# Optimization experiments

Measured on AMD Instinct MI355X. Metric: run time of the kernel, lower is better.

Reference implementation:

```python
import jax, jax.numpy as jnp
import numpy as np
from functools import partial

EPS = 1e-8

@partial(jax.custom_vjp, nondiff_argnums=(2, 3))
def ste_quantize(x, scale, clamp_min, clamp_max):
    # forward: clamp(round(x/scale), min, max); backward: grad/scale (STE)
    return jnp.clip(jnp.round(x / scale), clamp_min, clamp_max)

def _ste_fwd(x, scale, clamp_min, clamp_max):
    return ste_quantize(x, scale, clamp_min, clamp_max), scale

def _ste_bwd(clamp_min, clamp_max, scale, g):
    return (g / scale, jnp.zeros_like(scale))

ste_quantize.defvjp(_ste_fwd, _ste_bwd)


def setup_inputs() -> dict:
    key = jax.random.key(0)
    kx, kw = jax.random.split(key)
    x = jax.random.normal(kx, (4, 4096, 2048), dtype=jnp.float32)
    # nn.init.normal_(weight, mean=0.0, std=0.006)
    weight = 0.006 * jax.random.normal(kw, (2048, 2048), dtype=jnp.float32)
    return {"x": x, "weight": weight}


def reference(x, weight):
    # per-tensor ternary weight quantization: alpha = mean(|W|)
    alpha = jnp.maximum(jnp.mean(jnp.abs(weight)), EPS)
    w_q = ste_quantize(weight, alpha, -1.0, 1.0)  # (out, in), values in {-1,0,1}
    # per-token int8 activation quantization: beta = max(|x|)/127
    beta = jnp.maximum(jnp.max(jnp.abs(x), axis=-1, keepdims=True) / 127.0, EPS)  # (b,s,1)
    x_q = ste_quantize(x, beta, -127.0, 127.0)  # (b,s,in)
    # fp32 GEMM on quantized values, then dequant rescale
    y = jnp.einsum('bsi,oi->bso', x_q, w_q)
    return y * alpha * beta
```

## Files before the change

kernel.cpp:

```cpp
#include <hip/hip_runtime.h>

#define IN_DIM 2048
#define OUT_DIM 2048
#define EPS 1e-8f

#define BK 128
#define NKT (IN_DIM / BK)
#define HALF 16384

using int32x4 = __attribute__((ext_vector_type(4))) int;

__global__ __launch_bounds__(256) void prep_kernel(const float* __restrict__ x,
                                                   signed char* __restrict__ xq,
                                                   float* __restrict__ beta_arr,
                                                   int tokens,
                                                   const float* __restrict__ w,
                                                   double* __restrict__ sum, int n4) {
    if (blockIdx.x < 4096) {
        const int lane = threadIdx.x & 63;
        const int wave = threadIdx.x >> 6;
        const int t = blockIdx.x * 4 + wave;
        if (t >= tokens) return;
        const float4* row = (const float4*)(x + (size_t)t * IN_DIM);
        float4 v[8];
        float m = 0.f;
#pragma unroll
        for (int j = 0; j < 8; ++j) {
            v[j] = row[lane + 64 * j];
            m = fmaxf(m, fmaxf(fmaxf(fabsf(v[j].x), fabsf(v[j].y)),
                               fmaxf(fabsf(v[j].z), fabsf(v[j].w))));
        }
#pragma unroll
        for (int off = 32; off; off >>= 1) m = fmaxf(m, __shfl_xor(m, off));
        const float beta = fmaxf(m * (1.f / 127.f), EPS);
        if (lane == 0) beta_arr[t] = beta;
        char4* orow = (char4*)(xq + (size_t)t * IN_DIM);
#pragma unroll
        for (int j = 0; j < 8; ++j) {
            char4 q;
            q.x = (signed char)fminf(fmaxf(rintf(v[j].x / beta), -127.f), 127.f);
            q.y = (signed char)fminf(fmaxf(rintf(v[j].y / beta), -127.f), 127.f);
            q.z = (signed char)fminf(fmaxf(rintf(v[j].z / beta), -127.f), 127.f);
            q.w = (signed char)fminf(fmaxf(rintf(v[j].w / beta), -127.f), 127.f);
            orow[lane + 64 * j] = q;
        }
    } else {
        int tid = (blockIdx.x - 4096) * blockDim.x + threadIdx.x;
        int stride = 1024 * blockDim.x;
        float s = 0.f;
        for (int i = tid; i < n4; i += stride) {
            float4 vv = ((const float4*)w)[i];
            s += fabsf(vv.x) + fabsf(vv.y) + fabsf(vv.z) + fabsf(vv.w);
        }
        for (int off = 32; off; off >>= 1) s += __shfl_down(s, off);
        __shared__ float wsum[4];
        int lane = threadIdx.x & 63, wave = threadIdx.x >> 6;
        if (lane == 0) wsum[wave] = s;
        __syncthreads();
        if (threadIdx.x == 0) {
            double tt = (double)wsum[0] + (double)wsum[1] + (double)wsum[2] + (double)wsum[3];
            atomicAdd(sum, tt);
        }
    }
}

__global__ __launch_bounds__(256) void quantw_kernel(const float* __restrict__ w,
                                                     const double* __restrict__ sumptr,
                                                     signed char* __restrict__ wq,
                                                     float* __restrict__ alpha_out, int n4) {
    float alpha = fmaxf((float)(*sumptr * (1.0 / (double)(IN_DIM * OUT_DIM))), EPS);
    int i = blockIdx.x * blockDim.x + threadIdx.x;
    if (i == 0) *alpha_out = alpha;
    if (i >= n4) return;
    float4 v = ((const float4*)w)[i];
    char4 q;
    q.x = (signed char)fminf(fmaxf(rintf(v.x / alpha), -1.f), 1.f);
    q.y = (signed char)fminf(fmaxf(rintf(v.y / alpha), -1.f), 1.f);
    q.z = (signed char)fminf(fmaxf(rintf(v.z / alpha), -1.f), 1.f);
    q.w = (signed char)fminf(fmaxf(rintf(v.w / alpha), -1.f), 1.f);
    ((char4*)wq)[i] = q;
}

__device__ __forceinline__ void gll(const signed char* g, signed char* l) {
    __builtin_amdgcn_global_load_lds((const __attribute__((address_space(1))) void*)g,
        (__attribute__((address_space(3))) void*)l, 16, 0, 0);
}

#define CLUSTER(BASE, AF)                                                                      \
    __builtin_amdgcn_s_setprio(1);                                                             \
    _Pragma("unroll")                                                                          \
    for (int m_ = 0; m_ < 4; ++m_)                                                             \
        _Pragma("unroll")                                                                      \
        for (int n_ = 0; n_ < 4; ++n_)                                                         \
            acc[(BASE) + m_][n_] = __builtin_amdgcn_mfma_i32_16x16x64_i8(                      \
                AF[m_], bf[n_], acc[(BASE) + m_][n_], 0, 0, 0);                                \
    __builtin_amdgcn_s_setprio(0);

template<bool STG, bool TAIL>
__device__ __forceinline__ void ktile(int T, signed char* lds, int32x4 (&acc)[8][4],
                                      int aoff, int boff, int f0, int f1,
                                      const signed char* a0, const signed char* a1,
                                      const signed char* b0, const signed char* b1) {
    const int s = (T & 1) * HALF;
    const int d = ((T + 1) & 1) * HALF;
    const size_t ko = (size_t)(T + 1) * BK;
    int32x4 af0[4], af1[4], bf[4];

#pragma unroll
    for (int m = 0; m < 4; ++m) af0[m] = *(const int32x4*)(lds + s + aoff + m * 1024);
#pragma unroll
    for (int n = 0; n < 4; ++n) bf[n] = *(const int32x4*)(lds + 65536 + s + boff + n * 1024);
    if constexpr (STG) { gll(a0 + ko, lds + d + f0); gll(a1 + ko, lds + d + f1); }
#pragma unroll
    for (int m = 0; m < 4; ++m) af1[m] = *(const int32x4*)(lds + s + aoff + 4096 + m * 1024);
    CLUSTER(0, af0)
    if constexpr (STG) { gll(b0 + ko, lds + 65536 + d + f0); gll(b1 + ko, lds + 65536 + d + f1); }
    CLUSTER(4, af1)
    if constexpr (TAIL) asm volatile("s_waitcnt vmcnt(0)" ::: "memory");
    else                asm volatile("s_waitcnt vmcnt(4)" ::: "memory");
    __builtin_amdgcn_s_barrier();

#pragma unroll
    for (int m = 0; m < 4; ++m) af0[m] = *(const int32x4*)(lds + 32768 + s + aoff + m * 1024);
#pragma unroll
    for (int n = 0; n < 4; ++n) bf[n] = *(const int32x4*)(lds + 98304 + s + boff + n * 1024);
    if constexpr (STG) { gll(a0 + ko + 64, lds + 32768 + d + f0); gll(a1 + ko + 64, lds + 32768 + d + f1); }
#pragma unroll
    for (int m = 0; m < 4; ++m) af1[m] = *(const int32x4*)(lds + 32768 + s + aoff + 4096 + m * 1024);
    CLUSTER(0, af0)
    if constexpr (STG) { gll(b0 + ko + 64, lds + 98304 + d + f0); gll(b1 + ko + 64, lds + 98304 + d + f1); }
    CLUSTER(4, af1)
    if constexpr (!TAIL) {
        asm volatile("s_waitcnt vmcnt(4)" ::: "memory");
        __builtin_amdgcn_s_barrier();
    }
}

__global__ __launch_bounds__(512, 2) void gemm_kernel(const signed char* __restrict__ xq,
                                                      const signed char* __restrict__ wq,
                                                      const float* __restrict__ beta,
                                                      const float* __restrict__ alpha_p,
                                                      float* __restrict__ out) {
    extern __shared__ signed char lds[];
    const int tid = threadIdx.x;
    const int lane = tid & 63;
    const int wave = tid >> 6;
    const int wm = wave >> 2;
    const int wn = wave & 3;
    const int row0 = blockIdx.x * 256;
    const int col0 = blockIdx.y * 256;

    const int f0 = tid * 16;
    const int f1 = f0 + 8192;
    const int g0 = f0 >> 10, kg0 = (f0 >> 8) & 3, r0 = (f0 >> 4) & 15;
    const int g1 = f1 >> 10, kg1 = (f1 >> 8) & 3, r1 = (f1 >> 4) & 15;
    const signed char* a0 = xq + (size_t)(row0 + g0 * 16 + r0) * IN_DIM + kg0 * 16;
    const signed char* a1 = xq + (size_t)(row0 + g1 * 16 + r1) * IN_DIM + kg1 * 16;
    const signed char* b0 = wq + (size_t)(col0 + g0 * 16 + r0) * IN_DIM + kg0 * 16;
    const signed char* b1 = wq + (size_t)(col0 + g1 * 16 + r1) * IN_DIM + kg1 * 16;

    const int kr = (lane >> 4) * 256 + (lane & 15) * 16;
    const int aoff = wm * 8192 + kr;
    const int boff = wn * 4096 + kr;

    int32x4 acc[8][4] = {};

    gll(a0, lds + f0);              gll(a1, lds + f1);
    gll(b0, lds + 65536 + f0);      gll(b1, lds + 65536 + f1);
    gll(a0 + 64, lds + 32768 + f0); gll(a1 + 64, lds + 32768 + f1);
    gll(b0 + 64, lds + 98304 + f0); gll(b1 + 64, lds + 98304 + f1);
    asm volatile("s_waitcnt vmcnt(4)" ::: "memory");
    __builtin_amdgcn_s_barrier();

    for (int T = 0; T < NKT - 1; ++T)
        ktile<true, false>(T, lds, acc, aoff, boff, f0, f1, a0, a1, b0, b1);
    ktile<false, true>(NKT - 1, lds, acc, aoff, boff, f0, f1, a0, a1, b0, b1);

    const float alpha = *alpha_p;
#pragma unroll
    for (int mi = 0; mi < 8; ++mi) {
        int rbase = row0 + wm * 128 + mi * 16 + ((lane >> 4) << 2);
#pragma unroll
        for (int r = 0; r < 4; ++r) {
            int row = rbase + r;
            float scale = alpha * beta[row];
#pragma unroll
            for (int n = 0; n < 4; ++n) {
                int col = col0 + wn * 64 + n * 16 + (lane & 15);
                out[(size_t)row * OUT_DIM + col] = (float)acc[mi][n][r] * scale;
            }
        }
    }
}

extern "C" void kernel_launch(void* const* d_in, const int* in_sizes, int n_in,
                              void* d_out, int out_size, void* d_ws, size_t ws_size,
                              hipStream_t stream) {
    const float* x = (const float*)d_in[0];
    const float* w = (const float*)d_in[1];
    float* out = (float*)d_out;

    const int tokens = in_sizes[0] / IN_DIM;
    const int n_w = in_sizes[1];
    const int n_w4 = n_w / 4;

    char* ws = (char*)d_ws;
    double* d_sum = (double*)ws;
    float* d_alpha = (float*)(ws + 8);
    float* d_beta = (float*)(ws + 256);
    signed char* d_wq = (signed char*)(ws + 256 + 65536);
    signed char* d_xq = d_wq + (size_t)n_w;

    hipMemsetAsync(d_ws, 0, 16, stream);

    prep_kernel<<<5120, 256, 0, stream>>>(x, d_xq, d_beta, tokens, w, d_sum, n_w4);
    quantw_kernel<<<(n_w4 + 255) / 256, 256, 0, stream>>>(w, d_sum, d_wq, d_alpha, n_w4);

    hipFuncSetAttribute((const void*)gemm_kernel,
                        hipFuncAttributeMaxDynamicSharedMemorySize, 131072);

    dim3 grid(16384 / 256, OUT_DIM / 256);
    gemm_kernel<<<grid, 512, 131072, stream>>>(d_xq, d_wq, d_beta, d_alpha, out);
}
```

Measured before the change: 139.2 us.

## Fuse weight ternary quantization into prep kernel via grid-wide atomic barrier

Removes the separate quantw kernel launch. The 1024 weight-sum blocks now bump an atomic counter after adding their partial sums, spin until every block has arrived, compute alpha, and then quantize their own slice of the weight matrix in the same kernel. This saves one kernel launch and the gap between kernels. In exchange it depends on all 1024 abs-sum blocks being resident at once; they are launched after 4096 token blocks, so the spin-wait could stall or deadlock if the scheduler does not give them co-residency.

```diff
diff --git a/kernel.cpp b/kernel.cpp
--- a/kernel.cpp
+++ b/kernel.cpp
@@ -7,6 +7,8 @@
 #define BK 128
 #define NKT (IN_DIM / BK)
 #define HALF 16384
+
+#define NABS 1024
 
 using int32x4 = __attribute__((ext_vector_type(4))) int;
 
@@ -15,7 +17,10 @@
                                                    float* __restrict__ beta_arr,
                                                    int tokens,
                                                    const float* __restrict__ w,
-                                                   double* __restrict__ sum, int n4) {
+                                                   double* __restrict__ sum,
+                                                   unsigned* __restrict__ counter,
+                                                   signed char* __restrict__ wq,
+                                                   float* __restrict__ alpha_out, int n4) {
     if (blockIdx.x < 4096) {
         const int lane = threadIdx.x & 63;
         const int wave = threadIdx.x >> 6;
@@ -45,40 +50,45 @@
             orow[lane + 64 * j] = q;
         }
     } else {
-        int tid = (blockIdx.x - 4096) * blockDim.x + threadIdx.x;
-        int stride = 1024 * blockDim.x;
+        const int b = blockIdx.x - 4096;
+        int tid = b * 256 + threadIdx.x;
         float s = 0.f;
-        for (int i = tid; i < n4; i += stride) {
+        for (int i = tid; i < n4; i += NABS * 256) {
             float4 vv = ((const float4*)w)[i];
             s += fabsf(vv.x) + fabsf(vv.y) + fabsf(vv.z) + fabsf(vv.w);
         }
         for (int off = 32; off; off >>= 1) s += __shfl_down(s, off);
         __shared__ float wsum[4];
+        __shared__ float sh_alpha;
         int lane = threadIdx.x & 63, wave = threadIdx.x >> 6;
         if (lane == 0) wsum[wave] = s;
         __syncthreads();
         if (threadIdx.x == 0) {
             double tt = (double)wsum[0] + (double)wsum[1] + (double)wsum[2] + (double)wsum[3];
             atomicAdd(sum, tt);
+            __threadfence();
+            __hip_atomic_fetch_add(counter, 1u, __ATOMIC_ACQ_REL, __HIP_MEMORY_SCOPE_AGENT);
+            while (__hip_atomic_load(counter, __ATOMIC_ACQUIRE, __HIP_MEMORY_SCOPE_AGENT) < NABS)
+                __builtin_amdgcn_s_sleep(8);
+            double sv = __hip_atomic_load(sum, __ATOMIC_ACQUIRE, __HIP_MEMORY_SCOPE_AGENT);
+            float a = fmaxf((float)(sv * (1.0 / (double)(IN_DIM * OUT_DIM))), EPS);
+            sh_alpha = a;
+            if (b == 0) *alpha_out = a;
+        }
+        __syncthreads();
+        const float alpha = sh_alpha;
+#pragma unroll
+        for (int j = 0; j < 4; ++j) {
+            int i = b * 1024 + j * 256 + threadIdx.x;
+            float4 v = ((const float4*)w)[i];
+            char4 q;
+            q.x = (signed char)fminf(fmaxf(rintf(v.x / alpha), -1.f), 1.f);
+            q.y = (signed char)fminf(fmaxf(rintf(v.y / alpha), -1.f), 1.f);
+            q.z = (signed char)fminf(fmaxf(rintf(v.z / alpha), -1.f), 1.f);
+            q.w = (signed char)fminf(fmaxf(rintf(v.w / alpha), -1.f), 1.f);
+            ((char4*)wq)[i] = q;
         }
     }
-}
-
-__global__ __launch_bounds__(256) void quantw_kernel(const float* __restrict__ w,
-                                                     const double* __restrict__ sumptr,
-                                                     signed char* __restrict__ wq,
-                                                     float* __restrict__ alpha_out, int n4) {
-    float alpha = fmaxf((float)(*sumptr * (1.0 / (double)(IN_DIM * OUT_DIM))), EPS);
-    int i = blockIdx.x * blockDim.x + threadIdx.x;
-    if (i == 0) *alpha_out = alpha;
-    if (i >= n4) return;
-    float4 v = ((const float4*)w)[i];
-    char4 q;
-    q.x = (signed char)fminf(fmaxf(rintf(v.x / alpha), -1.f), 1.f);
-    q.y = (signed char)fminf(fmaxf(rintf(v.y / alpha), -1.f), 1.f);
-    q.z = (signed char)fminf(fmaxf(rintf(v.z / alpha), -1.f), 1.f);
-    q.w = (signed char)fminf(fmaxf(rintf(v.w / alpha), -1.f), 1.f);
-    ((char4*)wq)[i] = q;
 }
 
 __device__ __forceinline__ void gll(const signed char* g, signed char* l) {
@@ -207,14 +217,15 @@
     char* ws = (char*)d_ws;
     double* d_sum = (double*)ws;
     float* d_alpha = (float*)(ws + 8);
+    unsigned* d_cnt = (unsigned*)(ws + 16);
     float* d_beta = (float*)(ws + 256);
     signed char* d_wq = (signed char*)(ws + 256 + 65536);
     signed char* d_xq = d_wq + (size_t)n_w;
 
-    hipMemsetAsync(d_ws, 0, 16, stream);
-
-    prep_kernel<<<5120, 256, 0, stream>>>(x, d_xq, d_beta, tokens, w, d_sum, n_w4);
-    quantw_kernel<<<(n_w4 + 255) / 256, 256, 0, stream>>>(w, d_sum, d_wq, d_alpha, n_w4);
+    hipMemsetAsync(d_ws, 0, 32, stream);
+
+    prep_kernel<<<4096 + NABS, 256, 0, stream>>>(x, d_xq, d_beta, tokens,
+                                                 w, d_sum, d_cnt, d_wq, d_alpha, n_w4);
 
     hipFuncSetAttribute((const void*)gemm_kernel,
                         hipFuncAttributeMaxDynamicSharedMemorySize, 131072);
```

Result: slower. 262.4 us (+88.5%).

## Switch GEMM k-loop to triple-buffered LDS ring with 64-wide k tiles

Applied to the files above, without the earlier changes.

Replaces the double-buffered 128-wide k-tile pipeline with a three-slot LDS ring of 64-wide tiles. Global-to-LDS loads are issued two tiles ahead, and each step waits only for the older tile's loads. The goal is to hide global memory latency better and cut total LDS use from 128KB to 96KB. In exchange, loop-carried slot indices and runtime branches on the tail iterations are added.

```diff
diff --git a/kernel.cpp b/kernel.cpp
--- a/kernel.cpp
+++ b/kernel.cpp
@@ -4,9 +4,10 @@
 #define OUT_DIM 2048
 #define EPS 1e-8f
 
-#define BK 128
-#define NKT (IN_DIM / BK)
-#define HALF 16384
+#define BK 64
+#define NT (IN_DIM / BK)
+#define SLOT 32768
+#define LDS_SZ 98304
 
 using int32x4 = __attribute__((ext_vector_type(4))) int;
 
@@ -96,46 +97,6 @@
                 AF[m_], bf[n_], acc[(BASE) + m_][n_], 0, 0, 0);                                \
     __builtin_amdgcn_s_setprio(0);
 
-template<bool STG, bool TAIL>
-__device__ __forceinline__ void ktile(int T, signed char* lds, int32x4 (&acc)[8][4],
-                                      int aoff, int boff, int f0, int f1,
-                                      const signed char* a0, const signed char* a1,
-                                      const signed char* b0, const signed char* b1) {
-    const int s = (T & 1) * HALF;
-    const int d = ((T + 1) & 1) * HALF;
-    const size_t ko = (size_t)(T + 1) * BK;
-    int32x4 af0[4], af1[4], bf[4];
-
-#pragma unroll
-    for (int m = 0; m < 4; ++m) af0[m] = *(const int32x4*)(lds + s + aoff + m * 1024);
-#pragma unroll
-    for (int n = 0; n < 4; ++n) bf[n] = *(const int32x4*)(lds + 65536 + s + boff + n * 1024);
-    if constexpr (STG) { gll(a0 + ko, lds + d + f0); gll(a1 + ko, lds + d + f1); }
-#pragma unroll
-    for (int m = 0; m < 4; ++m) af1[m] = *(const int32x4*)(lds + s + aoff + 4096 + m * 1024);
-    CLUSTER(0, af0)
-    if constexpr (STG) { gll(b0 + ko, lds + 65536 + d + f0); gll(b1 + ko, lds + 65536 + d + f1); }
-    CLUSTER(4, af1)
-    if constexpr (TAIL) asm volatile("s_waitcnt vmcnt(0)" ::: "memory");
-    else                asm volatile("s_waitcnt vmcnt(4)" ::: "memory");
-    __builtin_amdgcn_s_barrier();
-
-#pragma unroll
-    for (int m = 0; m < 4; ++m) af0[m] = *(const int32x4*)(lds + 32768 + s + aoff + m * 1024);
-#pragma unroll
-    for (int n = 0; n < 4; ++n) bf[n] = *(const int32x4*)(lds + 98304 + s + boff + n * 1024);
-    if constexpr (STG) { gll(a0 + ko + 64, lds + 32768 + d + f0); gll(a1 + ko + 64, lds + 32768 + d + f1); }
-#pragma unroll
-    for (int m = 0; m < 4; ++m) af1[m] = *(const int32x4*)(lds + 32768 + s + aoff + 4096 + m * 1024);
-    CLUSTER(0, af0)
-    if constexpr (STG) { gll(b0 + ko + 64, lds + 98304 + d + f0); gll(b1 + ko + 64, lds + 98304 + d + f1); }
-    CLUSTER(4, af1)
-    if constexpr (!TAIL) {
-        asm volatile("s_waitcnt vmcnt(4)" ::: "memory");
-        __builtin_amdgcn_s_barrier();
-    }
-}
-
 __global__ __launch_bounds__(512, 2) void gemm_kernel(const signed char* __restrict__ xq,
                                                       const signed char* __restrict__ wq,
                                                       const float* __restrict__ beta,
@@ -161,20 +122,43 @@
 
     const int kr = (lane >> 4) * 256 + (lane & 15) * 16;
     const int aoff = wm * 8192 + kr;
-    const int boff = wn * 4096 + kr;
+    const int boff = 16384 + wn * 4096 + kr;
 
     int32x4 acc[8][4] = {};
 
-    gll(a0, lds + f0);              gll(a1, lds + f1);
-    gll(b0, lds + 65536 + f0);      gll(b1, lds + 65536 + f1);
-    gll(a0 + 64, lds + 32768 + f0); gll(a1 + 64, lds + 32768 + f1);
-    gll(b0 + 64, lds + 98304 + f0); gll(b1 + 64, lds + 98304 + f1);
+    gll(a0, lds + f0);                gll(a1, lds + f1);
+    gll(b0, lds + 16384 + f0);        gll(b1, lds + 16384 + f1);
+    gll(a0 + BK, lds + SLOT + f0);    gll(a1 + BK, lds + SLOT + f1);
+    gll(b0 + BK, lds + SLOT + 16384 + f0); gll(b1 + BK, lds + SLOT + 16384 + f1);
     asm volatile("s_waitcnt vmcnt(4)" ::: "memory");
     __builtin_amdgcn_s_barrier();
 
-    for (int T = 0; T < NKT - 1; ++T)
-        ktile<true, false>(T, lds, acc, aoff, boff, f0, f1, a0, a1, b0, b1);
-    ktile<false, true>(NKT - 1, lds, acc, aoff, boff, f0, f1, a0, a1, b0, b1);
+    int s = 0, d = 2;
+    for (int T = 0; T < NT; ++T) {
+        const signed char* ls = lds + s * SLOT;
+        signed char* ld = lds + d * SLOT;
+        const int ko = (T + 2) * BK;
+        int32x4 af0[4], af1[4], bf[4];
+#pragma unroll
+        for (int m = 0; m < 4; ++m) af0[m] = *(const int32x4*)(ls + aoff + m * 1024);
+#pragma unroll
+        for (int n = 0; n < 4; ++n) bf[n] = *(const int32x4*)(ls + boff + n * 1024);
+        if (T < NT - 2) { gll(a0 + ko, ld + f0); gll(a1 + ko, ld + f1); }
+#pragma unroll
+        for (int m = 0; m < 4; ++m) af1[m] = *(const int32x4*)(ls + aoff + 4096 + m * 1024);
+        CLUSTER(0, af0)
+        if (T < NT - 2) { gll(b0 + ko, ld + 16384 + f0); gll(b1 + ko, ld + 16384 + f1); }
+        CLUSTER(4, af1)
+        if (T < NT - 2) {
+            asm volatile("s_waitcnt vmcnt(4)" ::: "memory");
+            __builtin_amdgcn_s_barrier();
+        } else if (T == NT - 2) {
+            asm volatile("s_waitcnt vmcnt(0)" ::: "memory");
+            __builtin_amdgcn_s_barrier();
+        }
+        s = (s == 2) ? 0 : s + 1;
+        d = (d == 2) ? 0 : d + 1;
+    }
 
     const float alpha = *alpha_p;
 #pragma unroll
@@ -217,8 +201,8 @@
     quantw_kernel<<<(n_w4 + 255) / 256, 256, 0, stream>>>(w, d_sum, d_wq, d_alpha, n_w4);
 
     hipFuncSetAttribute((const void*)gemm_kernel,
-                        hipFuncAttributeMaxDynamicSharedMemorySize, 131072);
+                        hipFuncAttributeMaxDynamicSharedMemorySize, LDS_SZ);
 
     dim3 grid(16384 / 256, OUT_DIM / 256);
-    gemm_kernel<<<grid, 512, 131072, stream>>>(d_xq, d_wq, d_beta, d_alpha, out);
-}
+    gemm_kernel<<<grid, 512, LDS_SZ, stream>>>(d_xq, d_wq, d_beta, d_alpha, out);
+}
```

Result: no change. 139.6 us (+0.3%).
